# Kernel optimization log

Measured on AMD Instinct MI355X. Metric: run time of the kernel, lower is better.

## Reference

```python
import jax, jax.numpy as jnp
import numpy as np

L1, L2, B, D = 512, 512, 32, 768
EPS = 1e-8

def setup_inputs() -> dict:
    key = jax.random.key(0)
    k1, k2 = jax.random.split(key)
    return {
        "x1": jax.random.normal(k1, (L1, B, D), dtype=jnp.float32),
        "x1_mask": jnp.ones((L1, B), dtype=jnp.float32),
        "x2": jax.random.normal(k2, (L2, B, D), dtype=jnp.float32),
        "x2_mask": jnp.ones((L2, B), dtype=jnp.float32),
    }

def reference(x1, x1_mask, x2, x2_mask):
    # to batch-major: [B, L, D]
    x1b = jnp.transpose(x1, (1, 0, 2))
    x2b = jnp.transpose(x2, (1, 0, 2))
    m1 = jnp.transpose(x1_mask, (1, 0))  # [B, L1]
    m2 = jnp.transpose(x2_mask, (1, 0))  # [B, L2]

    # raw scores [B, L1, L2]
    scores = jnp.einsum('bld,bmd->blm', x1b, x2b)

    # x1 attends over x2: softmax over axis 2 with x2 mask
    w2 = jnp.exp(scores - jnp.max(scores, axis=2, keepdims=True))
    w2 = w2 * m2[:, None, :]
    alpha = w2 / (jnp.sum(w2, axis=-1, keepdims=True) + EPS)  # [B, L1, L2]
    x1_dual = jnp.einsum('blm,bmd->bld', alpha, x2b)           # [B, L1, D]

    # x2 attends over x1: stabilize with max over axis 1, then transpose
    w1 = jnp.exp(scores - jnp.max(scores, axis=1, keepdims=True))
    w1 = jnp.transpose(w1, (0, 2, 1))                          # [B, L2, L1]
    w1 = w1 * m1[:, None, :]
    beta = w1 / (jnp.sum(w1, axis=-1, keepdims=True) + EPS)    # [B, L2, L1]
    x2_dual = jnp.einsum('bml,bld->bmd', beta, x1b)            # [B, L2, D]

    # back to seq-major [L, B, D]
    return (jnp.transpose(x1_dual, (1, 0, 2)), jnp.transpose(x2_dual, (1, 0, 2)))
```

## Files before the change

### kernel.cpp

```cpp
#include <hip/hip_runtime.h>

#define LQ  512
#define LKN 512
#define BB  32
#define DD  768

typedef float    f4     __attribute__((ext_vector_type(4)));
typedef _Float16 half8  __attribute__((ext_vector_type(8)));
typedef _Float16 half4  __attribute__((ext_vector_type(4)));
typedef __fp16   fp16x2 __attribute__((ext_vector_type(2)));

union H8 { half8 h; unsigned int u[4]; };

__device__ __forceinline__ unsigned int pk2(float a, float b) {
    union { fp16x2 h; unsigned int u; } c;
    c.h = __builtin_amdgcn_cvt_pkrtz(a, b);
    return c.u;
}
__device__ __forceinline__ half8 cvt8(f4 a, f4 b) {
    H8 r;
    r.u[0] = pk2(a[0], a[1]); r.u[1] = pk2(a[2], a[3]);
    r.u[2] = pk2(b[0], b[1]); r.u[3] = pk2(b[2], b[3]);
    return r.h;
}

__device__ __forceinline__ void gload16(half8& dst, const _Float16* p) {
    asm volatile("global_load_dwordx4 %0, %1, off" : "=v"(dst) : "v"(p));
}
__device__ __forceinline__ void gloadf4(f4& dst, const float* p) {
    asm volatile("global_load_dwordx4 %0, %1, off" : "=v"(dst) : "v"(p));
}

__global__ __launch_bounds__(256)
void prep_pack(const float* __restrict__ x1, const float* __restrict__ x2,
               _Float16* __restrict__ xf1, _Float16* __restrict__ xf2,
               _Float16* __restrict__ xv1, _Float16* __restrict__ xv2)
{
    const int bi   = blockIdx.x;
    const int side = bi / 1536;
    const int rem  = bi % 1536;
    const int b    = rem / 48;
    const int rem2 = rem % 48;
    const int l0   = (rem2 / 6) * 64;
    const int d0   = (rem2 % 6) * 128;

    const float* __restrict__ X  = side ? x2  : x1;
    _Float16* __restrict__    XF = side ? xf2 : xf1;
    _Float16* __restrict__    XV = side ? xv2 : xv1;

    __shared__ _Float16 T[64][136];

    const int tid = threadIdx.x;
    {
        const int r  = tid >> 4;
        const int c8 = (tid & 15) * 8;
        const float* src = X + ((size_t)(l0 + r) * BB + b) * DD + d0 + c8;
        f4 v[8];
        #pragma unroll
        for (int k = 0; k < 4; ++k) {
            gloadf4(v[2 * k],     src + (size_t)k * 16 * BB * DD);
            gloadf4(v[2 * k + 1], src + (size_t)k * 16 * BB * DD + 4);
        }
        asm volatile("s_waitcnt vmcnt(4)" ::: "memory");
        __builtin_amdgcn_sched_barrier(0);
        #pragma unroll
        for (int k = 0; k < 2; ++k) {
            half4 ha, hb;
            ha[0] = (_Float16)v[2*k][0]; ha[1] = (_Float16)v[2*k][1];
            ha[2] = (_Float16)v[2*k][2]; ha[3] = (_Float16)v[2*k][3];
            hb[0] = (_Float16)v[2*k+1][0]; hb[1] = (_Float16)v[2*k+1][1];
            hb[2] = (_Float16)v[2*k+1][2]; hb[3] = (_Float16)v[2*k+1][3];
            *(half4*)&T[r + 16 * k][c8]     = ha;
            *(half4*)&T[r + 16 * k][c8 + 4] = hb;
        }
        asm volatile("s_waitcnt vmcnt(0)" ::: "memory");
        __builtin_amdgcn_sched_barrier(0);
        #pragma unroll
        for (int k = 2; k < 4; ++k) {
            half4 ha, hb;
            ha[0] = (_Float16)v[2*k][0]; ha[1] = (_Float16)v[2*k][1];
            ha[2] = (_Float16)v[2*k][2]; ha[3] = (_Float16)v[2*k][3];
            hb[0] = (_Float16)v[2*k+1][0]; hb[1] = (_Float16)v[2*k+1][1];
            hb[2] = (_Float16)v[2*k+1][2]; hb[3] = (_Float16)v[2*k+1][3];
            *(half4*)&T[r + 16 * k][c8]     = ha;
            *(half4*)&T[r + 16 * k][c8 + 4] = hb;
        }
    }
    __syncthreads();
    #pragma unroll
    for (int c2 = tid; c2 < 1024; c2 += 256) {
        const int dhalf = c2 >> 9;
        const int t16l  = (c2 >> 7) & 3;
        const int ksl   = (c2 >> 6) & 1;
        const int ln    = c2 & 63;
        half8 v = *(const half8*)&T[t16l * 16 + (ln & 15)][dhalf * 64 + ksl * 32 + (ln >> 4) * 8];
        const size_t t16g = (size_t)(l0 >> 4) + t16l;
        const size_t ksg  = (size_t)(d0 >> 5) + dhalf * 2 + ksl;
        *(half8*)(XF + (((size_t)b * 32 + t16g) * 24 + ksg) * 512 + ln * 8) = v;
    }
    #pragma unroll
    for (int c2 = tid; c2 < 1024; c2 += 256) {
        const int dtl  = c2 >> 7;
        const int ks2l = (c2 >> 6) & 1;
        const int ln   = c2 & 63;
        half8 v;
        #pragma unroll
        for (int jj = 0; jj < 8; ++jj)
            v[jj] = T[ks2l * 32 + (ln >> 4) * 8 + jj][dtl * 16 + (ln & 15)];
        const size_t dtg  = (size_t)(d0 >> 4) + dtl;
        const size_t ks2g = (size_t)(l0 >> 5) + ks2l;
        *(half8*)(XV + (((size_t)b * 48 + dtg) * 16 + ks2g) * 512 + ln * 8) = v;
    }
}

__global__ __launch_bounds__(256, 3)
void gemm_s(const _Float16* __restrict__ xf1, const _Float16* __restrict__ xf2,
            float* __restrict__ S)
{
    const int i   = blockIdx.x;
    const int xcd = i & 7;
    const int j   = i >> 3;
    const int t   = j & 15;
    const int b   = xcd * 4 + (j >> 4);
    const int lt  = t >> 2, mt = t & 3;
    const int l0b = lt * 128, m0b = mt * 128;

    const int tid  = threadIdx.x;
    const int lane = tid & 63;
    const int w    = tid >> 6;
    const int wl   = w >> 1, wm = w & 1;
    const int lr   = lane & 15;
    const int lg   = lane >> 4;

    f4 acc[16];
    #pragma unroll
    for (int t2 = 0; t2 < 16; ++t2) acc[t2] = f4{0.f, 0.f, 0.f, 0.f};

    {
        const _Float16* ab = xf1 + (((size_t)b * 32 + lt * 8 + wl * 4) * 24) * 512 + lane * 8;
        const _Float16* bb = xf2 + (((size_t)b * 32 + mt * 8 + wm * 4) * 24) * 512 + lane * 8;
        __builtin_amdgcn_s_setprio(1);
        #pragma unroll
        for (int ks = 0; ks < 24; ++ks) {
            half8 aF[4], bF[4];
            #pragma unroll
            for (int q = 0; q < 4; ++q) {
                aF[q] = *(const half8*)(ab + ((size_t)q * 24 + ks) * 512);
                bF[q] = *(const half8*)(bb + ((size_t)q * 24 + ks) * 512);
            }
            #pragma unroll
            for (int q = 0; q < 4; ++q)
                #pragma unroll
                for (int p = 0; p < 4; ++p)
                    acc[q * 4 + p] = __builtin_amdgcn_mfma_f32_16x16x32_f16(aF[q], bF[p], acc[q * 4 + p], 0, 0, 0);
        }
        __builtin_amdgcn_s_setprio(0);
    }

    {
        float* srow = S + ((size_t)b * 512 + l0b + wl * 64) * 512 + m0b + wm * 64;
        #pragma unroll
        for (int q = 0; q < 4; ++q)
            #pragma unroll
            for (int p = 0; p < 4; ++p)
                #pragma unroll
                for (int r = 0; r < 4; ++r)
                    srow[(size_t)(q * 16 + 4 * lg + r) * 512 + p * 16 + lr] = acc[q * 4 + p][r];
    }
}

__global__ __launch_bounds__(256)
void softmax_both(const float* __restrict__ S32, float* __restrict__ PF0,
                  float* __restrict__ PF1,
                  const float* __restrict__ m1, const float* __restrict__ m2)
{
    const int bi   = blockIdx.x;
    const int side = bi >> 9;
    const int idx  = bi & 511;
    const int b    = idx >> 4;
    const int t    = idx & 15;

    const int tid  = threadIdx.x;

    if (side == 0) {
        const int lane = tid & 63;
        const int w    = tid >> 6;
        __shared__ float mask_r[LKN];
        mask_r[tid] = m2[tid * BB + b];
        mask_r[tid + 256] = m2[(tid + 256) * BB + b];
        __syncthreads();

        float mk[8];
        #pragma unroll
        for (int j = 0; j < 8; ++j) mk[j] = mask_r[lane * 8 + j];

        const int row0 = t * 32 + w * 8;

        f4 fa[8], fb[8];
        #pragma unroll
        for (int rr = 0; rr < 8; ++rr) {
            const float* rp = S32 + ((size_t)b * 512 + row0 + rr) * 512 + lane * 8;
            fa[rr] = *(const f4*)rp;
            fb[rr] = *(const f4*)(rp + 4);
        }

        #pragma unroll
        for (int rr = 0; rr < 8; ++rr) {
            float f[8] = {fa[rr][0], fa[rr][1], fa[rr][2], fa[rr][3],
                          fb[rr][0], fb[rr][1], fb[rr][2], fb[rr][3]};
            float m = fmaxf(fmaxf(fmaxf(f[0], f[1]), fmaxf(f[2], f[3])),
                            fmaxf(fmaxf(f[4], f[5]), fmaxf(f[6], f[7])));
            #pragma unroll
            for (int d = 1; d <= 32; d <<= 1) m = fmaxf(m, __shfl_xor(m, d));
            float e[8], s = 0.f;
            #pragma unroll
            for (int j = 0; j < 8; ++j) { e[j] = __expf(f[j] - m) * mk[j]; s += e[j]; }
            #pragma unroll
            for (int d = 1; d <= 32; d <<= 1) s += __shfl_xor(s, d);
            const float inv = 1.f / (s + 1e-8f);
            H8 o;
            o.u[0] = pk2(e[0] * inv, e[1] * inv); o.u[1] = pk2(e[2] * inv, e[3] * inv);
            o.u[2] = pk2(e[4] * inv, e[5] * inv); o.u[3] = pk2(e[6] * inv, e[7] * inv);
            const int row = row0 + rr;
            char* base = (char*)PF0 + ((size_t)b * 32 + (row >> 4)) * 16384;
            *(half8*)(base + (lane >> 2) * 1024 + (lane & 3) * 256 + (row & 15) * 16) = o.h;
        }
    } else {
        __shared__ float raw[32][513];
        __shared__ float mask_c[LKN];
        __shared__ float redm[8][32];
        __shared__ float reds[8][32];

        mask_c[tid] = m1[tid * BB + b];
        mask_c[tid + 256] = m1[(tid + 256) * BB + b];

        {
            const float* sbase = S32 + ((size_t)b * 512 + (tid >> 3)) * 512 + t * 32 + (tid & 7) * 4;
            f4 vv[16];
            #pragma unroll
            for (int it = 0; it < 8; ++it) gloadf4(vv[it], sbase + (size_t)it * 32 * 512);
            asm volatile("s_waitcnt vmcnt(0)" ::: "memory");
            __builtin_amdgcn_sched_barrier(0);
            #pragma unroll
            for (int it = 8; it < 16; ++it) gloadf4(vv[it], sbase + (size_t)it * 32 * 512);
            #pragma unroll
            for (int it = 0; it < 8; ++it) {
                const int row = it * 32 + (tid >> 3);
                const int c0  = (tid & 7) * 4;
                raw[c0 + 0][row] = vv[it][0]; raw[c0 + 1][row] = vv[it][1];
                raw[c0 + 2][row] = vv[it][2]; raw[c0 + 3][row] = vv[it][3];
            }
            asm volatile("s_waitcnt vmcnt(0)" ::: "memory");
            __builtin_amdgcn_sched_barrier(0);
            #pragma unroll
            for (int it = 8; it < 16; ++it) {
                const int row = it * 32 + (tid >> 3);
                const int c0  = (tid & 7) * 4;
                raw[c0 + 0][row] = vv[it][0]; raw[c0 + 1][row] = vv[it][1];
                raw[c0 + 2][row] = vv[it][2]; raw[c0 + 3][row] = vv[it][3];
            }
        }
        __syncthreads();

        const int col = tid & 31;
        const int seg = tid >> 5;

        float m = -3.0e38f;
        #pragma unroll
        for (int r = 0; r < 64; ++r) m = fmaxf(m, raw[col][seg * 64 + r]);
        redm[seg][col] = m;
        __syncthreads();
        float M = redm[0][col];
        #pragma unroll
        for (int s2 = 1; s2 < 8; ++s2) M = fmaxf(M, redm[s2][col]);

        float s = 0.f;
        #pragma unroll
        for (int r = 0; r < 64; ++r) {
            const int row = seg * 64 + r;
            s += __expf(raw[col][row] - M) * mask_c[row];
        }
        reds[seg][col] = s;
        __syncthreads();
        float L = 0.f;
        #pragma unroll
        for (int s2 = 0; s2 < 8; ++s2) L += reds[s2][col];
        const float inv = 1.f / (L + 1e-8f);

        const int col_g = t * 32 + col;
        char* pfb = (char*)PF1 + ((size_t)b * 32 + (col_g >> 4)) * 16384;
        #pragma unroll
        for (int kc = 0; kc < 8; ++kc) {
            const int k0 = seg * 64 + kc * 8;
            float e[8];
            #pragma unroll
            for (int j = 0; j < 8; ++j)
                e[j] = __expf(raw[col][k0 + j] - M) * mask_c[k0 + j] * inv;
            H8 o;
            o.u[0] = pk2(e[0], e[1]); o.u[1] = pk2(e[2], e[3]);
            o.u[2] = pk2(e[4], e[5]); o.u[3] = pk2(e[6], e[7]);
            const int lw = seg * 8 + kc;
            *(half8*)(pfb + (lw >> 2) * 1024 + (lw & 3) * 256 + (col_g & 15) * 16) = o.h;
        }
    }
}

__global__ __launch_bounds__(256)
void pv_frag(const float* __restrict__ PF0, const float* __restrict__ PF1,
             const _Float16* __restrict__ xv1, const _Float16* __restrict__ xv2,
             float* __restrict__ o1, float* __restrict__ o2)
{
    const int i    = blockIdx.x;
    const int xcd  = i & 7;
    const int j    = i >> 3;
    const int lt   = j & 7;
    const int dq   = (j >> 3) & 3;
    const int side = (j >> 5) & 1;
    const int b    = xcd * 4 + (j >> 6);
    const int l0   = lt * 64;

    const float* __restrict__ PF    = side ? PF1 : PF0;
    const _Float16* __restrict__ VF = side ? xv1 : xv2;
    float* __restrict__ OUT         = side ? o2 : o1;

    const int tid  = threadIdx.x;
    const int lane = tid & 63;
    const int w    = tid >> 6;
    const int lr   = lane & 15;
    const int lg   = lane >> 4;

    const char* pb[4];
    #pragma unroll
    for (int q = 0; q < 4; ++q)
        pb[q] = (const char*)PF + ((size_t)b * 32 + lt * 4 + q) * 16384 + lane * 16;
    const _Float16* vbase = VF + (((size_t)b * 48 + dq * 12 + w * 3) * 16) * 512 + lane * 8;

    f4 acc[12];
    #pragma unroll
    for (int t = 0; t < 12; ++t) acc[t] = f4{0.f, 0.f, 0.f, 0.f};

    half8 pa[2][2][4], vf[2][2][3];

    #pragma unroll
    for (int k2 = 0; k2 < 2; ++k2) {
        #pragma unroll
        for (int q = 0; q < 4; ++q)
            gload16(pa[0][k2][q], (const _Float16*)(pb[q] + k2 * 1024));
        #pragma unroll
        for (int nt = 0; nt < 3; ++nt)
            gload16(vf[0][k2][nt], vbase + ((size_t)nt * 16 + k2) * 512);
    }

    #pragma unroll
    for (int cb = 0; cb < 8; ++cb) {
        const int cur = cb & 1;
        const int nxt = cur ^ 1;
        if (cb < 7) {
            #pragma unroll
            for (int k2 = 0; k2 < 2; ++k2) {
                const int ks2 = (cb + 1) * 2 + k2;
                #pragma unroll
                for (int q = 0; q < 4; ++q)
                    gload16(pa[nxt][k2][q], (const _Float16*)(pb[q] + ks2 * 1024));
                #pragma unroll
                for (int nt = 0; nt < 3; ++nt)
                    gload16(vf[nxt][k2][nt], vbase + ((size_t)nt * 16 + ks2) * 512);
            }
            asm volatile("s_waitcnt vmcnt(14)" ::: "memory");
        } else {
            asm volatile("s_waitcnt vmcnt(0)" ::: "memory");
        }
        __builtin_amdgcn_sched_barrier(0);
        __builtin_amdgcn_s_setprio(1);
        #pragma unroll
        for (int k2 = 0; k2 < 2; ++k2)
            #pragma unroll
            for (int nt = 0; nt < 3; ++nt)
                #pragma unroll
                for (int q = 0; q < 4; ++q)
                    acc[q * 3 + nt] = __builtin_amdgcn_mfma_f32_16x16x32_f16(pa[cur][k2][q], vf[cur][k2][nt], acc[q * 3 + nt], 0, 0, 0);
        __builtin_amdgcn_s_setprio(0);
    }

    #pragma unroll
    for (int q = 0; q < 4; ++q)
        #pragma unroll
        for (int nt = 0; nt < 3; ++nt)
            #pragma unroll
            for (int r = 0; r < 4; ++r)
                OUT[((size_t)(l0 + q * 16 + 4 * lg + r) * BB + b) * DD + dq * 192 + (w * 3 + nt) * 16 + lr]
                    = acc[q * 3 + nt][r];
}

__global__ __launch_bounds__(256)
void coatt_flash_f32(const float* __restrict__ x1, const float* __restrict__ m1,
                     const float* __restrict__ x2, const float* __restrict__ m2,
                     float* __restrict__ o1, float* __restrict__ o2)
{
    const int i    = blockIdx.x;
    const int xcd  = i & 7;
    const int j    = i >> 3;
    const int pair = xcd * 8 + (j >> 5);
    const int qt   = j & 31;
    const int side = pair >> 5;
    const int b    = pair & 31;

    const float* __restrict__ Q   = side ? x2 : x1;
    const float* __restrict__ K   = side ? x1 : x2;
    const float* __restrict__ MK  = side ? m1 : m2;
    float* __restrict__       OUT = side ? o2 : o1;

    const int tid  = threadIdx.x;
    const int lane = tid & 63;
    const int w    = tid >> 6;
    const int lr   = lane & 15;
    const int lg   = lane >> 4;
    const int q0 = qt * 16;
    const int d0 = w * (DD / 4);

    __shared__ float sred[4][16][36];
    __shared__ float mask_s[LKN];
    for (int t = tid; t < LKN; t += 256) mask_s[t] = MK[t * BB + b];

    half8 qf[6];
    {
        const float* qrow = Q + ((q0 + lr) * BB + b) * DD + d0 + lg * 8;
        #pragma unroll
        for (int ks = 0; ks < 6; ++ks) {
            f4 a = *(const f4*)(qrow + ks * 32);
            f4 c = *(const f4*)(qrow + ks * 32 + 4);
            qf[ks] = cvt8(a, c);
        }
    }
    f4 acc[12];
    #pragma unroll
    for (int t = 0; t < 12; ++t) acc[t] = f4{0.f, 0.f, 0.f, 0.f};
    float Mrun = -3.0e38f, Lrun = 0.f;
    for (int kt = 0; kt < 16; ++kt) {
        const int k0 = kt * 32;
        f4 s0 = {0.f,0.f,0.f,0.f}, s1 = {0.f,0.f,0.f,0.f};
        {
            const float* kb0 = K + ((k0 + lr) * BB + b) * DD + d0 + lg * 8;
            const float* kb1 = kb0 + 16 * BB * DD;
            #pragma unroll
            for (int ks = 0; ks < 6; ++ks) {
                f4 a0 = *(const f4*)(kb0 + ks * 32);
                f4 c0 = *(const f4*)(kb0 + ks * 32 + 4);
                s0 = __builtin_amdgcn_mfma_f32_16x16x32_f16(qf[ks], cvt8(a0, c0), s0, 0, 0, 0);
                f4 a1 = *(const f4*)(kb1 + ks * 32);
                f4 c1 = *(const f4*)(kb1 + ks * 32 + 4);
                s1 = __builtin_amdgcn_mfma_f32_16x16x32_f16(qf[ks], cvt8(a1, c1), s1, 0, 0, 0);
            }
        }
        __syncthreads();
        #pragma unroll
        for (int r = 0; r < 4; ++r) {
            sred[w][4 * lg + r][lr]      = s0[r];
            sred[w][4 * lg + r][16 + lr] = s1[r];
        }
        __syncthreads();
        f4 sa = {0.f,0.f,0.f,0.f}, sb = {0.f,0.f,0.f,0.f};
        #pragma unroll
        for (int ww = 0; ww < 4; ++ww) {
            sa += *(const f4*)&sred[ww][lr][lg * 8];
            sb += *(const f4*)&sred[ww][lr][lg * 8 + 4];
        }
        float tmax = fmaxf(fmaxf(fmaxf(sa[0], sa[1]), fmaxf(sa[2], sa[3])),
                           fmaxf(fmaxf(sb[0], sb[1]), fmaxf(sb[2], sb[3])));
        tmax = fmaxf(tmax, __shfl_xor(tmax, 16));
        tmax = fmaxf(tmax, __shfl_xor(tmax, 32));
        const float Mnew  = fmaxf(Mrun, tmax);
        const float scale = __expf(Mrun - Mnew);
        float p[8];
        float psum = 0.f;
        const float* mrow = &mask_s[k0 + lg * 8];
        #pragma unroll
        for (int t = 0; t < 4; ++t) { p[t]     = __expf(sa[t] - Mnew) * mrow[t];     psum += p[t]; }
        #pragma unroll
        for (int t = 0; t < 4; ++t) { p[4 + t] = __expf(sb[t] - Mnew) * mrow[4 + t]; psum += p[4 + t]; }
        psum += __shfl_xor(psum, 16);
        psum += __shfl_xor(psum, 32);
        Lrun = Lrun * scale + psum;
        Mrun = Mnew;
        H8 pf;
        pf.u[0] = pk2(p[0], p[1]); pf.u[1] = pk2(p[2], p[3]);
        pf.u[2] = pk2(p[4], p[5]); pf.u[3] = pk2(p[6], p[7]);
        float sc[4];
        #pragma unroll
        for (int r = 0; r < 4; ++r) sc[r] = __shfl(scale, (lane & 48) + 4 * lg + r);
        #pragma unroll
        for (int t = 0; t < 12; ++t) {
            acc[t][0] *= sc[0]; acc[t][1] *= sc[1];
            acc[t][2] *= sc[2]; acc[t][3] *= sc[3];
        }
        const float* vb = K + ((k0 + lg * 8) * BB + b) * DD + d0 + lr;
        #pragma unroll
        for (int nt = 0; nt < 12; ++nt) {
            const float* vp = vb + nt * 16;
            float vv[8];
            #pragma unroll
            for (int t = 0; t < 8; ++t) vv[t] = vp[t * BB * DD];
            H8 vf;
            vf.u[0] = pk2(vv[0], vv[1]); vf.u[1] = pk2(vv[2], vv[3]);
            vf.u[2] = pk2(vv[4], vv[5]); vf.u[3] = pk2(vv[6], vv[7]);
            acc[nt] = __builtin_amdgcn_mfma_f32_16x16x32_f16(pf.h, vf.h, acc[nt], 0, 0, 0);
        }
    }
    float il[4];
    {
        const float inv = 1.f / (Lrun + 1e-8f);
        #pragma unroll
        for (int r = 0; r < 4; ++r) il[r] = __shfl(inv, (lane & 48) + 4 * lg + r);
    }
    #pragma unroll
    for (int nt = 0; nt < 12; ++nt) {
        #pragma unroll
        for (int r = 0; r < 4; ++r) {
            OUT[((q0 + 4 * lg + r) * BB + b) * DD + d0 + nt * 16 + lr] = acc[nt][r] * il[r];
        }
    }
}

extern "C" void kernel_launch(void* const* d_in, const int* in_sizes, int n_in,
                              void* d_out, int out_size, void* d_ws, size_t ws_size,
                              hipStream_t stream) {
    (void)in_sizes; (void)n_in; (void)out_size;
    const float* x1 = (const float*)d_in[0];
    const float* m1 = (const float*)d_in[1];
    const float* x2 = (const float*)d_in[2];
    const float* m2 = (const float*)d_in[3];
    float* o1 = (float*)d_out;
    float* o2 = o1 + (size_t)LQ * BB * DD;

    const size_t ELEMS = (size_t)LQ * BB * DD;
    const size_t SELEM = (size_t)BB * 512 * 512;
    const size_t NEED  = 4 * ELEMS * sizeof(_Float16)
                       + SELEM * sizeof(float);

    if (ws_size >= NEED) {
        _Float16* xf1 = (_Float16*)d_ws;
        _Float16* xf2 = xf1 + ELEMS;
        _Float16* xv1 = xf2 + ELEMS;
        _Float16* xv2 = xv1 + ELEMS;
        float*    S32 = (float*)(xv2 + ELEMS);
        float*    PF0 = (float*)d_ws;
        float*    PF1 = (float*)((char*)d_ws + (size_t)32 * 32 * 16384);
        prep_pack<<<3072, 256, 0, stream>>>(x1, x2, xf1, xf2, xv1, xv2);
        gemm_s<<<512, 256, 0, stream>>>(xf1, xf2, S32);
        softmax_both<<<1024, 256, 0, stream>>>(S32, PF0, PF1, m1, m2);
        pv_frag<<<2048, 256, 0, stream>>>(PF0, PF1, xv1, xv2, o1, o2);
    } else {
        coatt_flash_f32<<<2048, 256, 0, stream>>>(x1, m1, x2, m2, o1, o2);
    }
}
```

Before: 135.2 us.

## Split fp16 pack kernel into direct-store XF kernel and smaller-tile XV transpose kernel

Replaces the single prep_pack kernel with two kernels. prep_xf writes the MFMA fragment layout directly from global loads into registers without going through LDS. prep_xv handles only the transposed V layout, using 64x64 tiles and twice as many blocks. This removes LDS staging and synchronisation for the XF path, but reads the fp32 inputs twice and adds an extra kernel launch.

```diff
diff --git a/kernel.cpp b/kernel.cpp
--- a/kernel.cpp
+++ b/kernel.cpp
@@ -32,76 +32,86 @@
 }
 
 __global__ __launch_bounds__(256)
-void prep_pack(const float* __restrict__ x1, const float* __restrict__ x2,
-               _Float16* __restrict__ xf1, _Float16* __restrict__ xf2,
-               _Float16* __restrict__ xv1, _Float16* __restrict__ xv2)
+void prep_xf(const float* __restrict__ x1, const float* __restrict__ x2,
+             _Float16* __restrict__ xf1, _Float16* __restrict__ xf2)
 {
     const int bi   = blockIdx.x;
     const int side = bi / 1536;
-    const int rem  = bi % 1536;
-    const int b    = rem / 48;
-    const int rem2 = rem % 48;
-    const int l0   = (rem2 / 6) * 64;
-    const int d0   = (rem2 % 6) * 128;
+    const int blm  = bi % 1536;
+    const int b    = blm / 48;
+    const int rblk = blm % 48;
 
     const float* __restrict__ X  = side ? x2  : x1;
     _Float16* __restrict__    XF = side ? xf2 : xf1;
+
+    const int tid  = threadIdx.x;
+    const int lane = tid & 63;
+    const int wv   = tid >> 6;
+    const int lr   = lane & 15;
+    const int lg   = lane >> 4;
+
+    int r2[4];
+    const float* src[4];
+    #pragma unroll
+    for (int i = 0; i < 4; ++i) {
+        r2[i] = rblk * 16 + wv * 4 + i;
+        const int t16 = r2[i] / 24;
+        const int ks  = r2[i] - t16 * 24;
+        src[i] = X + ((size_t)(t16 * 16 + lr) * BB + b) * DD + ks * 32 + lg * 8;
+    }
+
+    f4 lo[4], hi[4];
+    #pragma unroll
+    for (int i = 0; i < 4; ++i) { gloadf4(lo[i], src[i]); gloadf4(hi[i], src[i] + 4); }
+    asm volatile("s_waitcnt vmcnt(0)" ::: "memory");
+    __builtin_amdgcn_sched_barrier(0);
+
+    #pragma unroll
+    for (int i = 0; i < 4; ++i)
+        *(half8*)(XF + ((size_t)b * 768 + r2[i]) * 512 + lane * 8) = cvt8(lo[i], hi[i]);
+}
+
+__global__ __launch_bounds__(256)
+void prep_xv(const float* __restrict__ x1, const float* __restrict__ x2,
+             _Float16* __restrict__ xv1, _Float16* __restrict__ xv2)
+{
+    const int bi   = blockIdx.x;
+    const int side = bi / 3072;
+    const int rem  = bi % 3072;
+    const int b    = rem / 96;
+    const int rem2 = rem % 96;
+    const int l0   = (rem2 / 12) * 64;
+    const int d0   = (rem2 % 12) * 64;
+
+    const float* __restrict__ X  = side ? x2  : x1;
     _Float16* __restrict__    XV = side ? xv2 : xv1;
 
-    __shared__ _Float16 T[64][136];
+    __shared__ _Float16 T[64][72];
 
     const int tid = threadIdx.x;
     {
-        const int r  = tid >> 4;
-        const int c8 = (tid & 15) * 8;
-        const float* src = X + ((size_t)(l0 + r) * BB + b) * DD + d0 + c8;
-        f4 v[8];
-        #pragma unroll
-        for (int k = 0; k < 4; ++k) {
-            gloadf4(v[2 * k],     src + (size_t)k * 16 * BB * DD);
-            gloadf4(v[2 * k + 1], src + (size_t)k * 16 * BB * DD + 4);
-        }
-        asm volatile("s_waitcnt vmcnt(4)" ::: "memory");
-        __builtin_amdgcn_sched_barrier(0);
-        #pragma unroll
-        for (int k = 0; k < 2; ++k) {
-            half4 ha, hb;
-            ha[0] = (_Float16)v[2*k][0]; ha[1] = (_Float16)v[2*k][1];
-            ha[2] = (_Float16)v[2*k][2]; ha[3] = (_Float16)v[2*k][3];
-            hb[0] = (_Float16)v[2*k+1][0]; hb[1] = (_Float16)v[2*k+1][1];
-            hb[2] = (_Float16)v[2*k+1][2]; hb[3] = (_Float16)v[2*k+1][3];
-            *(half4*)&T[r + 16 * k][c8]     = ha;
-            *(half4*)&T[r + 16 * k][c8 + 4] = hb;
-        }
+        const int r  = tid >> 2;
+        const int c0 = (tid & 3) * 16;
+        const float* src = X + ((size_t)(l0 + r) * BB + b) * DD + d0 + c0;
+        f4 v[4];
+        #pragma unroll
+        for (int k = 0; k < 4; ++k) gloadf4(v[k], src + k * 4);
         asm volatile("s_waitcnt vmcnt(0)" ::: "memory");
         __builtin_amdgcn_sched_barrier(0);
         #pragma unroll
-        for (int k = 2; k < 4; ++k) {
-            half4 ha, hb;
-            ha[0] = (_Float16)v[2*k][0]; ha[1] = (_Float16)v[2*k][1];
-            ha[2] = (_Float16)v[2*k][2]; ha[3] = (_Float16)v[2*k][3];
-            hb[0] = (_Float16)v[2*k+1][0]; hb[1] = (_Float16)v[2*k+1][1];
-            hb[2] = (_Float16)v[2*k+1][2]; hb[3] = (_Float16)v[2*k+1][3];
-            *(half4*)&T[r + 16 * k][c8]     = ha;
-            *(half4*)&T[r + 16 * k][c8 + 4] = hb;
+        for (int k = 0; k < 4; ++k) {
+            half4 h;
+            h[0] = (_Float16)v[k][0]; h[1] = (_Float16)v[k][1];
+            h[2] = (_Float16)v[k][2]; h[3] = (_Float16)v[k][3];
+            *(half4*)&T[r][c0 + k * 4] = h;
         }
     }
     __syncthreads();
     #pragma unroll
-    for (int c2 = tid; c2 < 1024; c2 += 256) {
-        const int dhalf = c2 >> 9;
-        const int t16l  = (c2 >> 7) & 3;
-        const int ksl   = (c2 >> 6) & 1;
-        const int ln    = c2 & 63;
-        half8 v = *(const half8*)&T[t16l * 16 + (ln & 15)][dhalf * 64 + ksl * 32 + (ln >> 4) * 8];
-        const size_t t16g = (size_t)(l0 >> 4) + t16l;
-        const size_t ksg  = (size_t)(d0 >> 5) + dhalf * 2 + ksl;
-        *(half8*)(XF + (((size_t)b * 32 + t16g) * 24 + ksg) * 512 + ln * 8) = v;
-    }
-    #pragma unroll
-    for (int c2 = tid; c2 < 1024; c2 += 256) {
-        const int dtl  = c2 >> 7;
-        const int ks2l = (c2 >> 6) & 1;
+    for (int c2 = tid; c2 < 512; c2 += 256) {
+        const int g    = c2 >> 6;
+        const int dtl  = g >> 1;
+        const int ks2l = g & 1;
         const int ln   = c2 & 63;
         half8 v;
         #pragma unroll
@@ -545,7 +555,8 @@
         float*    S32 = (float*)(xv2 + ELEMS);
         float*    PF0 = (float*)d_ws;
         float*    PF1 = (float*)((char*)d_ws + (size_t)32 * 32 * 16384);
-        prep_pack<<<3072, 256, 0, stream>>>(x1, x2, xf1, xf2, xv1, xv2);
+        prep_xf<<<3072, 256, 0, stream>>>(x1, x2, xf1, xf2);
+        prep_xv<<<6144, 256, 0, stream>>>(x1, x2, xv1, xv2);
         gemm_s<<<512, 256, 0, stream>>>(xf1, xf2, S32);
         softmax_both<<<1024, 256, 0, stream>>>(S32, PF0, PF1, m1, m2);
         pv_frag<<<2048, 256, 0, stream>>>(PF0, PF1, xv1, xv2, o1, o2);
```

New measurement: 150.3 us. +11.2%, slower.
